# Kernel optimization log

Hardware: AMD Instinct MI355X
Metric: run time of the kernel (lower is better)

The kernel has to match this reference:

```python
import jax, jax.numpy as jnp
import numpy as np

HEADS = 8
DIM_HEAD = 64
WINDOW = 8  # local_window_size


def _sn_weight(W, u, sigma):
    """SNLinear reparameterized weight: one power-iteration step (detached)
    then sigma_W = v^T W u (grad flows through W only), weight = W/sigma_W * sigma."""
    v = W @ u
    v = v / jnp.linalg.norm(v)
    u2 = W.T @ v
    u2 = u2 / jnp.linalg.norm(u2)
    v = jax.lax.stop_gradient(v)
    u2 = jax.lax.stop_gradient(u2)
    sigma_w = jnp.einsum('c,cd,d->', v, W, u2)
    return W / sigma_w * sigma


def setup_inputs() -> dict:
    key = jax.random.key(0)
    ks = jax.random.split(key, 6)
    B, S, D = 2, 2048, 512
    inner = HEADS * DIM_HEAD  # 512
    x = jax.random.normal(ks[0], (B, S, D), dtype=jnp.float32)
    W_qkv = 0.02 * jax.random.normal(ks[1], (3 * inner, D), dtype=jnp.float32)
    u_qkv = jax.random.normal(ks[2], (D,), dtype=jnp.float32)
    u_qkv = u_qkv / jnp.linalg.norm(u_qkv)
    W_out = 0.02 * jax.random.normal(ks[3], (D, inner), dtype=jnp.float32)
    b_out = jnp.zeros((D,), dtype=jnp.float32)
    u_out = jax.random.normal(ks[4], (inner,), dtype=jnp.float32)
    u_out = u_out / jnp.linalg.norm(u_out)
    sigma_qkv = jnp.ones((1,), dtype=jnp.float32)
    sigma_out = jnp.ones((1,), dtype=jnp.float32)
    temperature = jnp.asarray(np.log(DIM_HEAD ** -0.5), dtype=jnp.float32)
    return {
        'x': x, 'W_qkv': W_qkv, 'u_qkv': u_qkv, 'sigma_qkv': sigma_qkv,
        'W_out': W_out, 'b_out': b_out, 'u_out': u_out, 'sigma_out': sigma_out,
        'temperature': temperature,
    }


def reference(x, W_qkv, u_qkv, sigma_qkv, W_out, b_out, u_out, sigma_out, temperature):
    B, S, D = x.shape
    # qkv projection (spectral-normed, no bias)
    Wq = _sn_weight(W_qkv, u_qkv, sigma_qkv[0])
    qkv = x @ Wq.T                                   # [B,S,3*inner]
    q, k, v = jnp.split(qkv, 3, axis=-1)
    to_heads = lambda t: t.reshape(B, S, HEADS, DIM_HEAD).transpose(0, 2, 1, 3)
    q, k, v = to_heads(q), to_heads(k), to_heads(v)   # [B,H,S,Dh]
    dots = jnp.einsum('bhid,bhjd->bhij', q, k) * jnp.exp(temperature)
    # local causal band mask (True inside band); original masked_fill fills True
    i = jnp.arange(S)
    band = (i[:, None] >= i[None, :]) & ((i[:, None] - i[None, :]) <= (WINDOW - 1))
    neg = -jnp.finfo(dots.dtype).max
    dots = jnp.where(band[None, None, :, :], neg, dots)
    attn = jax.nn.softmax(dots, axis=-1)
    out = jnp.einsum('bhij,bhjd->bhid', attn, v)      # [B,H,S,Dh]
    out = out.transpose(0, 2, 1, 3).reshape(B, S, HEADS * DIM_HEAD)
    Wo = _sn_weight(W_out, u_out, sigma_out[0])
    return out @ Wo.T + b_out
```

## Files before the change

kernel.cpp:

```cpp
#include <hip/hip_runtime.h>
#include <hip/hip_bf16.h>
#include <math.h>

#define HEADS 8
#define DH 64
#define SEQ 2048
#define BATCH 2
#define DMODEL 512
#define INNER 512
#define WIN 8

typedef unsigned short ushort_t;
typedef __attribute__((ext_vector_type(8))) __bf16 bf16x8;
typedef __attribute__((ext_vector_type(8))) unsigned short u16x8;
typedef __attribute__((ext_vector_type(4))) float f32x4;

__device__ inline float bf2f(ushort_t u) {
    unsigned v = ((unsigned)u) << 16; float f; __builtin_memcpy(&f, &v, 4); return f;
}
__device__ inline ushort_t f2bf(float f) {
    __hip_bfloat16 h = __float2bfloat16(f); ushort_t u; __builtin_memcpy(&u, &h, 2); return u;
}
__device__ inline int swz_idx(int row, int col) { return ((row << 6) | col) ^ ((row & 7) << 3); }

__device__ inline bf16x8 ld_frag(const ushort_t* lds, int row, int col) {
    u16x8 v = *(const u16x8*)&lds[swz_idx(row, col)];
    return __builtin_bit_cast(bf16x8, v);
}
__device__ inline f32x4 mfma16(bf16x8 a, bf16x8 b, f32x4 c) {
    return __builtin_amdgcn_mfma_f32_16x16x32_bf16(a, b, c, 0, 0, 0);
}
__device__ inline void gload16(const void* g, void* l) {
    __builtin_amdgcn_global_load_lds(
        (const __attribute__((address_space(1))) unsigned int*)g,
        (__attribute__((address_space(3))) unsigned int*)l, 16, 0, 0);
}

__global__ __launch_bounds__(256) void cast_zero_kernel(const float* __restrict__ x,
                                                        const float* __restrict__ Wq,
                                                        const float* __restrict__ Wo,
                                                        ushort_t* __restrict__ xb,
                                                        ushort_t* __restrict__ wqb,
                                                        ushort_t* __restrict__ wob,
                                                        float* __restrict__ zbuf) {
    const int gid = blockIdx.x * 256 + threadIdx.x;
    const float* src; ushort_t* dst; int g;
    if (gid < 262144)      { src = x;  dst = xb;  g = gid; }
    else if (gid < 360448) { src = Wq; dst = wqb; g = gid - 262144; }
    else                   { src = Wo; dst = wob; g = gid - 360448; }
    float4 a = *(const float4*)&src[(size_t)g * 8];
    float4 b = *(const float4*)&src[(size_t)g * 8 + 4];
    u16x8 o;
    o[0] = f2bf(a.x); o[1] = f2bf(a.y); o[2] = f2bf(a.z); o[3] = f2bf(a.w);
    o[4] = f2bf(b.x); o[5] = f2bf(b.y); o[6] = f2bf(b.z); o[7] = f2bf(b.w);
    *(u16x8*)&dst[(size_t)g * 8] = o;
    if (gid < 1024) zbuf[gid] = 0.f;
}

__global__ __launch_bounds__(256) void sn1_kernel(const float* __restrict__ Wq,
                                                  const float* __restrict__ uq,
                                                  const float* __restrict__ Wo,
                                                  const float* __restrict__ uo,
                                                  float* __restrict__ v1,
                                                  float* __restrict__ v2) {
    const int lane = threadIdx.x & 63, w = threadIdx.x >> 6;
    const int r = blockIdx.x * 4 + w;
    const float* W; const float* u; float* vout; int rr;
    if (r < 1536) { W = Wq; u = uq; vout = v1; rr = r; }
    else          { W = Wo; u = uo; vout = v2; rr = r - 1536; }
    float4 w0 = *(const float4*)&W[(size_t)rr * 512 + lane * 8];
    float4 w1 = *(const float4*)&W[(size_t)rr * 512 + lane * 8 + 4];
    float4 u0 = *(const float4*)&u[lane * 8];
    float4 u1 = *(const float4*)&u[lane * 8 + 4];
    float dot = w0.x * u0.x + w0.y * u0.y + w0.z * u0.z + w0.w * u0.w +
                w1.x * u1.x + w1.y * u1.y + w1.z * u1.z + w1.w * u1.w;
#pragma unroll
    for (int off = 1; off < 64; off <<= 1) dot += __shfl_xor(dot, off, 64);
    if (lane == 0) vout[rr] = dot;
}

__global__ __launch_bounds__(256) void sn2_kernel(const float* __restrict__ Wq,
                                                  const float* __restrict__ Wo,
                                                  const float* __restrict__ v1,
                                                  const float* __restrict__ v2,
                                                  float* __restrict__ z1,
                                                  float* __restrict__ z2) {
    const int t = threadIdx.x, b = blockIdx.x;
    const float* W; const float* v; float* z; int r0;
    if (b < 96) { W = Wq; v = v1; z = z1; r0 = b * 16; }
    else        { W = Wo; v = v2; z = z2; r0 = (b - 96) * 16; }
    float a0 = 0.f, a1 = 0.f;
    for (int i = 0; i < 16; ++i) {
        float vv = v[r0 + i];
        a0 += W[(size_t)(r0 + i) * 512 + t] * vv;
        a1 += W[(size_t)(r0 + i) * 512 + 256 + t] * vv;
    }
    atomicAdd(&z[t], a0);
    atomicAdd(&z[t + 256], a1);
}

__global__ __launch_bounds__(256) void sn3_kernel(const float* __restrict__ v1,
                                                  const float* __restrict__ v2,
                                                  const float* __restrict__ z1,
                                                  const float* __restrict__ z2,
                                                  const float* __restrict__ sq,
                                                  const float* __restrict__ so,
                                                  float* __restrict__ scales) {
    __shared__ float red[256];
    const int t = threadIdx.x;
    const float* v; const float* z; const float* sg; int R;
    if (blockIdx.x == 0) { v = v1; z = z1; sg = sq; R = 1536; }
    else                 { v = v2; z = z2; sg = so; R = 512;  }
    float n1 = 0.f;
    for (int i = t; i < R; i += 256) { float x = v[i]; n1 += x * x; }
    red[t] = n1; __syncthreads();
    for (int off = 128; off > 0; off >>= 1) { if (t < off) red[t] += red[t + off]; __syncthreads(); }
    n1 = red[0]; __syncthreads();
    float n2 = 0.f;
    for (int i = t; i < 512; i += 256) { float x = z[i]; n2 += x * x; }
    red[t] = n2; __syncthreads();
    for (int off = 128; off > 0; off >>= 1) { if (t < off) red[t] += red[t + off]; __syncthreads(); }
    if (t == 0) scales[blockIdx.x] = sg[0] * sqrtf(n1 / red[0]);
}

__global__ __launch_bounds__(256) void gemm_bt_qkv(const ushort_t* __restrict__ A,
                                                   const ushort_t* __restrict__ B,
                                                   ushort_t* __restrict__ qkv) {
    constexpr int K = DMODEL;
    __shared__ ushort_t As[8 * 128 * 8];
    __shared__ ushort_t Bs[8 * 128 * 8];
    const int t = threadIdx.x, lane = t & 63, w = t >> 6;
    const int wm = w >> 1, wn = w & 1, lg = lane >> 4, li = lane & 15;
    const int m0 = blockIdx.y * 128, n0 = blockIdx.x * 128;
    f32x4 acc[4][4] = {};
    for (int k0 = 0; k0 < K; k0 += 64) {
        __syncthreads();
#pragma unroll
        for (int i = 0; i < 4; ++i) {
            int j = w * 4 + i;
            int kc = j >> 1, mh = (j & 1) * 64;
            gload16(&A[(size_t)(m0 + mh + lane) * K + k0 + kc * 8], &As[(kc * 128 + mh) * 8]);
            gload16(&B[(size_t)(n0 + mh + lane) * K + k0 + kc * 8], &Bs[(kc * 128 + mh) * 8]);
        }
        __syncthreads();
#pragma unroll
        for (int kw = 0; kw < 2; ++kw) {
            bf16x8 af[4], bf[4];
#pragma unroll
            for (int mi = 0; mi < 4; ++mi)
                af[mi] = *(const bf16x8*)&As[((kw * 4 + lg) * 128 + wm * 64 + mi * 16 + li) * 8];
#pragma unroll
            for (int ni = 0; ni < 4; ++ni)
                bf[ni] = *(const bf16x8*)&Bs[((kw * 4 + lg) * 128 + wn * 64 + ni * 16 + li) * 8];
#pragma unroll
            for (int mi = 0; mi < 4; ++mi)
#pragma unroll
                for (int ni = 0; ni < 4; ++ni)
                    acc[mi][ni] = mfma16(af[mi], bf[ni], acc[mi][ni]);
        }
    }
    ushort_t* vT = qkv + (size_t)2 * BATCH * HEADS * SEQ * DH;
    if (n0 >= 1024) {
#pragma unroll
        for (int mi = 0; mi < 4; ++mi) {
            int base = m0 + wm * 64 + mi * 16 + lg * 4;
            int bb = base >> 11, ss = base & 2047;
#pragma unroll
            for (int ni = 0; ni < 4; ++ni) {
                int n = n0 + wn * 64 + ni * 16 + li;
                int h = (n >> 6) & 7, d0 = n & 63;
                ushort4 o;
                o.x = f2bf(acc[mi][ni][0]); o.y = f2bf(acc[mi][ni][1]);
                o.z = f2bf(acc[mi][ni][2]); o.w = f2bf(acc[mi][ni][3]);
                *(ushort4*)&vT[((size_t)((bb * HEADS + h) * DH) + d0) * SEQ + ss] = o;
            }
        }
    } else {
#pragma unroll
        for (int mi = 0; mi < 4; ++mi)
#pragma unroll
            for (int r = 0; r < 4; ++r) {
                int row = m0 + wm * 64 + mi * 16 + lg * 4 + r;
                int bb = row >> 11, ss = row & 2047;
#pragma unroll
                for (int ni = 0; ni < 4; ++ni) {
                    int n = n0 + wn * 64 + ni * 16 + li;
                    int which = n >> 9, h = (n >> 6) & 7, d0 = n & 63;
                    qkv[(size_t)which * (BATCH * HEADS * SEQ * DH) +
                        ((size_t)((bb * HEADS + h) * SEQ) + ss) * DH + d0] = f2bf(acc[mi][ni][r]);
                }
            }
    }
}

__global__ __launch_bounds__(256) void gemm_bt_out(const ushort_t* __restrict__ A,
                                                   const ushort_t* __restrict__ B,
                                                   const float* __restrict__ scales,
                                                   const float* __restrict__ bias,
                                                   float* __restrict__ C) {
    constexpr int K = INNER;
    __shared__ ushort_t As[8 * 128 * 8];
    __shared__ ushort_t Bs[8 * 128 * 8];
    const int t = threadIdx.x, lane = t & 63, w = t >> 6;
    const int wm = w >> 1, wn = w & 1, lg = lane >> 4, li = lane & 15;
    const int m0 = blockIdx.y * 128, n0 = blockIdx.x * 128;
    f32x4 acc[4][4] = {};
    for (int k0 = 0; k0 < K; k0 += 64) {
        __syncthreads();
#pragma unroll
        for (int i = 0; i < 4; ++i) {
            int j = w * 4 + i;
            int kc = j >> 1, mh = (j & 1) * 64;
            gload16(&A[(size_t)(m0 + mh + lane) * K + k0 + kc * 8], &As[(kc * 128 + mh) * 8]);
            gload16(&B[(size_t)(n0 + mh + lane) * K + k0 + kc * 8], &Bs[(kc * 128 + mh) * 8]);
        }
        __syncthreads();
#pragma unroll
        for (int kw = 0; kw < 2; ++kw) {
            bf16x8 af[4], bf[4];
#pragma unroll
            for (int mi = 0; mi < 4; ++mi)
                af[mi] = *(const bf16x8*)&As[((kw * 4 + lg) * 128 + wm * 64 + mi * 16 + li) * 8];
#pragma unroll
            for (int ni = 0; ni < 4; ++ni)
                bf[ni] = *(const bf16x8*)&Bs[((kw * 4 + lg) * 128 + wn * 64 + ni * 16 + li) * 8];
#pragma unroll
            for (int mi = 0; mi < 4; ++mi)
#pragma unroll
                for (int ni = 0; ni < 4; ++ni)
                    acc[mi][ni] = mfma16(af[mi], bf[ni], acc[mi][ni]);
        }
    }
    const float sc = scales[0] * scales[1];
#pragma unroll
    for (int mi = 0; mi < 4; ++mi)
#pragma unroll
        for (int r = 0; r < 4; ++r) {
            int row = m0 + wm * 64 + mi * 16 + lg * 4 + r;
#pragma unroll
            for (int ni = 0; ni < 4; ++ni) {
                int n = n0 + wn * 64 + ni * 16 + li;
                C[(size_t)row * INNER + n] = acc[mi][ni][r] * sc + bias[n];
            }
        }
}

__global__ __launch_bounds__(512) void attn_mfma_kernel(const ushort_t* __restrict__ qkv,
                                                        const float* __restrict__ temp,
                                                        const float* __restrict__ scales,
                                                        ushort_t* __restrict__ attn_out) {
    __shared__ ushort_t lds[6 * 4096];
    __shared__ float lsr[64];
    const int t    = threadIdx.x;
    const int lane = t & 63, w = t >> 6;
    const int g    = w >> 2, wl = w & 3;
    const int lg   = lane >> 4, li = lane & 15;
    const int bh   = blockIdx.x >> 5;
    const int i0   = (blockIdx.x & 31) * 64;
    const ushort_t* qp  = qkv;
    const ushort_t* kp  = qkv + (size_t)BATCH * HEADS * SEQ * DH;
    const ushort_t* vTp = kp  + (size_t)BATCH * HEADS * SEQ * DH;
    const float s0 = scales[0];
    const float st = expf(temp[0]) * s0 * s0;

    ushort_t* Kb = lds + g * 4096;
    ushort_t* Vb = lds + 8192 + g * 4096;
    ushort_t* Pb = lds + 16384 + g * 4096;

    bf16x8 aQ[2];
#pragma unroll
    for (int c = 0; c < 2; ++c) {
        u16x8 qv = *(const u16x8*)&qp[((size_t)bh * SEQ + i0 + 16 * wl + li) * DH + 32 * c + lg * 8];
        u16x8 r;
#pragma unroll
        for (int j = 0; j < 8; ++j) r[j] = f2bf(bf2f(qv[j]) * st);
        aQ[c] = __builtin_bit_cast(bf16x8, r);
    }

    float lsum[4] = {0.f, 0.f, 0.f, 0.f};
    f32x4 oacc[4] = {};

    for (int jt = 0; jt < SEQ / 128; ++jt) {
        __syncthreads();
        for (int u = t; u < 2048; u += 512) {
            int sel = u >> 9, idx = u & 511;
            int row = idx >> 3, ch = idx & 7;
            int j0s = (2 * jt + (sel & 1)) * 64;
            u16x8 val;
            if (sel < 2) val = *(const u16x8*)&kp[((size_t)bh * SEQ + j0s + row) * DH + ch * 8];
            else         val = *(const u16x8*)&vTp[((size_t)bh * DH + row) * SEQ + j0s + ch * 8];
            ushort_t* dst = lds + ((sel & 2) << 12) + ((sel & 1) << 12);
            *(u16x8*)&dst[swz_idx(row, ch * 8)] = val;
        }
        __syncthreads();

        const int j0 = (2 * jt + g) * 64;
        f32x4 s[4];
#pragma unroll
        for (int kc = 0; kc < 4; ++kc) {
            bf16x8 b0 = ld_frag(Kb, kc * 16 + li, lg * 8);
            bf16x8 b1 = ld_frag(Kb, kc * 16 + li, 32 + lg * 8);
            f32x4 z = {0.f, 0.f, 0.f, 0.f};
            z = mfma16(aQ[0], b0, z);
            z = mfma16(aQ[1], b1, z);
            s[kc] = z;
        }
        const bool need_mask = (j0 == i0) || (j0 == i0 - 64);
        if (need_mask) {
#pragma unroll
            for (int kc = 0; kc < 4; ++kc)
#pragma unroll
                for (int r = 0; r < 4; ++r) {
                    int qi = i0 + 16 * wl + lg * 4 + r;
                    int kj = j0 + kc * 16 + li;
                    float pv = ((unsigned)(qi - kj) < (unsigned)WIN) ? 0.f : __expf(s[kc][r]);
                    lsum[r] += pv;
                    Pb[swz_idx(16 * wl + lg * 4 + r, kc * 16 + li)] = f2bf(pv);
                }
        } else {
#pragma unroll
            for (int kc = 0; kc < 4; ++kc)
#pragma unroll
                for (int r = 0; r < 4; ++r) {
                    float pv = __expf(s[kc][r]);
                    lsum[r] += pv;
                    Pb[swz_idx(16 * wl + lg * 4 + r, kc * 16 + li)] = f2bf(pv);
                }
        }
        bf16x8 aP[2];
#pragma unroll
        for (int c = 0; c < 2; ++c) aP[c] = ld_frag(Pb, 16 * wl + li, c * 32 + lg * 8);
#pragma unroll
        for (int tt = 0; tt < 4; ++tt) {
            bf16x8 b0 = ld_frag(Vb, tt * 16 + li, lg * 8);
            bf16x8 b1 = ld_frag(Vb, tt * 16 + li, 32 + lg * 8);
            oacc[tt] = mfma16(aP[0], b0, oacc[tt]);
            oacc[tt] = mfma16(aP[1], b1, oacc[tt]);
        }
    }
#pragma unroll
    for (int r = 0; r < 4; ++r) {
        float l = lsum[r];
        l += __shfl_xor(l, 1, 16);
        l += __shfl_xor(l, 2, 16);
        l += __shfl_xor(l, 4, 16);
        l += __shfl_xor(l, 8, 16);
        lsum[r] = l;
    }
    float* O_part = (float*)lds;
    __syncthreads();
    if (g == 1) {
#pragma unroll
        for (int r = 0; r < 4; ++r) {
            int row = 16 * wl + lg * 4 + r;
            if (li == 0) lsr[row] = lsum[r];
#pragma unroll
            for (int tt = 0; tt < 4; ++tt)
                O_part[row * 64 + tt * 16 + li] = oacc[tt][r];
        }
    }
    __syncthreads();
    if (g == 0) {
        const int b_ = bh >> 3, h = bh & 7;
#pragma unroll
        for (int r = 0; r < 4; ++r) {
            int row = 16 * wl + lg * 4 + r;
            float inv = 1.0f / (lsum[r] + lsr[row]);
            size_t base = ((size_t)(b_ * SEQ + i0 + row)) * INNER + h * DH;
#pragma unroll
            for (int tt = 0; tt < 4; ++tt)
                attn_out[base + tt * 16 + li] =
                    f2bf((oacc[tt][r] + O_part[row * 64 + tt * 16 + li]) * inv);
        }
    }
}

extern "C" void kernel_launch(void* const* d_in, const int* in_sizes, int n_in,
                              void* d_out, int out_size, void* d_ws, size_t ws_size,
                              hipStream_t stream) {
    const float* x     = (const float*)d_in[0];
    const float* W_qkv = (const float*)d_in[1];
    const float* u_qkv = (const float*)d_in[2];
    const float* s_qkv = (const float*)d_in[3];
    const float* W_out = (const float*)d_in[4];
    const float* b_out = (const float*)d_in[5];
    const float* u_out = (const float*)d_in[6];
    const float* s_out = (const float*)d_in[7];
    const float* temp  = (const float*)d_in[8];
    float* out = (float*)d_out;

    float* scales = (float*)d_ws;
    float* v1 = scales + 64;
    float* v2 = v1 + 1536;
    float* z1 = v2 + 512;
    float* z2 = z1 + 512;
    ushort_t* xb    = (ushort_t*)((char*)d_ws + 16384);
    ushort_t* wqb   = xb + (size_t)2097152;
    ushort_t* wob   = wqb + (size_t)786432;
    ushort_t* qkvb  = wob + (size_t)262144;
    ushort_t* attnb = qkvb + (size_t)6291456;

    cast_zero_kernel<<<dim3(1536), dim3(256), 0, stream>>>(x, W_qkv, W_out, xb, wqb, wob, z1);
    sn1_kernel<<<dim3(512), dim3(256), 0, stream>>>(W_qkv, u_qkv, W_out, u_out, v1, v2);
    sn2_kernel<<<dim3(128), dim3(256), 0, stream>>>(W_qkv, W_out, v1, v2, z1, z2);
    sn3_kernel<<<dim3(2), dim3(256), 0, stream>>>(v1, v2, z1, z2, s_qkv, s_out, scales);
    gemm_bt_qkv<<<dim3(12, 32), dim3(256), 0, stream>>>(xb, wqb, qkvb);
    attn_mfma_kernel<<<dim3(512), dim3(512), 0, stream>>>(qkvb, temp, scales, attnb);
    gemm_bt_out<<<dim3(4, 32), dim3(256), 0, stream>>>(attnb, wob, scales, b_out, out);
}
```

Measured before the change: 173.6 us.

## Fuse spectral-norm prep kernels and double-buffer K/V tiles in attention

```diff
diff --git a/kernel.cpp b/kernel.cpp
--- a/kernel.cpp
+++ b/kernel.cpp
@@ -36,91 +36,97 @@
         (__attribute__((address_space(3))) unsigned int*)l, 16, 0, 0);
 }
 
-__global__ __launch_bounds__(256) void cast_zero_kernel(const float* __restrict__ x,
-                                                        const float* __restrict__ Wq,
-                                                        const float* __restrict__ Wo,
-                                                        ushort_t* __restrict__ xb,
-                                                        ushort_t* __restrict__ wqb,
-                                                        ushort_t* __restrict__ wob,
-                                                        float* __restrict__ zbuf) {
-    const int gid = blockIdx.x * 256 + threadIdx.x;
-    const float* src; ushort_t* dst; int g;
-    if (gid < 262144)      { src = x;  dst = xb;  g = gid; }
-    else if (gid < 360448) { src = Wq; dst = wqb; g = gid - 262144; }
-    else                   { src = Wo; dst = wob; g = gid - 360448; }
-    float4 a = *(const float4*)&src[(size_t)g * 8];
-    float4 b = *(const float4*)&src[(size_t)g * 8 + 4];
-    u16x8 o;
-    o[0] = f2bf(a.x); o[1] = f2bf(a.y); o[2] = f2bf(a.z); o[3] = f2bf(a.w);
-    o[4] = f2bf(b.x); o[5] = f2bf(b.y); o[6] = f2bf(b.z); o[7] = f2bf(b.w);
-    *(u16x8*)&dst[(size_t)g * 8] = o;
-    if (gid < 1024) zbuf[gid] = 0.f;
-}
-
-__global__ __launch_bounds__(256) void sn1_kernel(const float* __restrict__ Wq,
-                                                  const float* __restrict__ uq,
-                                                  const float* __restrict__ Wo,
-                                                  const float* __restrict__ uo,
-                                                  float* __restrict__ v1,
-                                                  float* __restrict__ v2) {
-    const int lane = threadIdx.x & 63, w = threadIdx.x >> 6;
-    const int r = blockIdx.x * 4 + w;
-    const float* W; const float* u; float* vout; int rr;
-    if (r < 1536) { W = Wq; u = uq; vout = v1; rr = r; }
-    else          { W = Wo; u = uo; vout = v2; rr = r - 1536; }
-    float4 w0 = *(const float4*)&W[(size_t)rr * 512 + lane * 8];
-    float4 w1 = *(const float4*)&W[(size_t)rr * 512 + lane * 8 + 4];
-    float4 u0 = *(const float4*)&u[lane * 8];
-    float4 u1 = *(const float4*)&u[lane * 8 + 4];
-    float dot = w0.x * u0.x + w0.y * u0.y + w0.z * u0.z + w0.w * u0.w +
-                w1.x * u1.x + w1.y * u1.y + w1.z * u1.z + w1.w * u1.w;
-#pragma unroll
-    for (int off = 1; off < 64; off <<= 1) dot += __shfl_xor(dot, off, 64);
-    if (lane == 0) vout[rr] = dot;
-}
-
-__global__ __launch_bounds__(256) void sn2_kernel(const float* __restrict__ Wq,
-                                                  const float* __restrict__ Wo,
-                                                  const float* __restrict__ v1,
-                                                  const float* __restrict__ v2,
-                                                  float* __restrict__ z1,
-                                                  float* __restrict__ z2) {
+__global__ __launch_bounds__(256) void fused_cast_sn1(const float* __restrict__ x,
+                                                      const float* __restrict__ Wq,
+                                                      const float* __restrict__ Wo,
+                                                      const float* __restrict__ uq,
+                                                      const float* __restrict__ uo,
+                                                      ushort_t* __restrict__ xb,
+                                                      ushort_t* __restrict__ wqb,
+                                                      ushort_t* __restrict__ wob,
+                                                      float* __restrict__ zbuf,
+                                                      float* __restrict__ v1,
+                                                      float* __restrict__ v2) {
+    const int b = blockIdx.x;
+    if (b < 1536) {
+        const int gid = b * 256 + threadIdx.x;
+        const float* src; ushort_t* dst; int g;
+        if (gid < 262144)      { src = x;  dst = xb;  g = gid; }
+        else if (gid < 360448) { src = Wq; dst = wqb; g = gid - 262144; }
+        else                   { src = Wo; dst = wob; g = gid - 360448; }
+        float4 a = *(const float4*)&src[(size_t)g * 8];
+        float4 c = *(const float4*)&src[(size_t)g * 8 + 4];
+        u16x8 o;
+        o[0] = f2bf(a.x); o[1] = f2bf(a.y); o[2] = f2bf(a.z); o[3] = f2bf(a.w);
+        o[4] = f2bf(c.x); o[5] = f2bf(c.y); o[6] = f2bf(c.z); o[7] = f2bf(c.w);
+        *(u16x8*)&dst[(size_t)g * 8] = o;
+        if (gid < 1032) zbuf[gid] = 0.f;
+    } else {
+        const int lane = threadIdx.x & 63, w = threadIdx.x >> 6;
+        const int r = (b - 1536) * 4 + w;
+        const float* W; const float* u; float* vout; int rr;
+        if (r < 1536) { W = Wq; u = uq; vout = v1; rr = r; }
+        else          { W = Wo; u = uo; vout = v2; rr = r - 1536; }
+        float4 w0 = *(const float4*)&W[(size_t)rr * 512 + lane * 8];
+        float4 w1 = *(const float4*)&W[(size_t)rr * 512 + lane * 8 + 4];
+        float4 u0 = *(const float4*)&u[lane * 8];
+        float4 u1 = *(const float4*)&u[lane * 8 + 4];
+        float dot = w0.x * u0.x + w0.y * u0.y + w0.z * u0.z + w0.w * u0.w +
+                    w1.x * u1.x + w1.y * u1.y + w1.z * u1.z + w1.w * u1.w;
+#pragma unroll
+        for (int off = 1; off < 64; off <<= 1) dot += __shfl_xor(dot, off, 64);
+        if (lane == 0) vout[rr] = dot;
+    }
+}
+
+__global__ __launch_bounds__(256) void fused_sn2_sn3(const float* __restrict__ Wq,
+                                                     const float* __restrict__ Wo,
+                                                     const float* __restrict__ v1,
+                                                     const float* __restrict__ v2,
+                                                     float* __restrict__ z1,
+                                                     float* __restrict__ z2,
+                                                     float* __restrict__ counter,
+                                                     const float* __restrict__ sq,
+                                                     const float* __restrict__ so,
+                                                     float* __restrict__ scales) {
+    __shared__ float red[256];
+    __shared__ int is_last;
     const int t = threadIdx.x, b = blockIdx.x;
-    const float* W; const float* v; float* z; int r0;
-    if (b < 96) { W = Wq; v = v1; z = z1; r0 = b * 16; }
-    else        { W = Wo; v = v2; z = z2; r0 = (b - 96) * 16; }
-    float a0 = 0.f, a1 = 0.f;
-    for (int i = 0; i < 16; ++i) {
-        float vv = v[r0 + i];
-        a0 += W[(size_t)(r0 + i) * 512 + t] * vv;
-        a1 += W[(size_t)(r0 + i) * 512 + 256 + t] * vv;
-    }
-    atomicAdd(&z[t], a0);
-    atomicAdd(&z[t + 256], a1);
-}
-
-__global__ __launch_bounds__(256) void sn3_kernel(const float* __restrict__ v1,
-                                                  const float* __restrict__ v2,
-                                                  const float* __restrict__ z1,
-                                                  const float* __restrict__ z2,
-                                                  const float* __restrict__ sq,
-                                                  const float* __restrict__ so,
-                                                  float* __restrict__ scales) {
-    __shared__ float red[256];
-    const int t = threadIdx.x;
-    const float* v; const float* z; const float* sg; int R;
-    if (blockIdx.x == 0) { v = v1; z = z1; sg = sq; R = 1536; }
-    else                 { v = v2; z = z2; sg = so; R = 512;  }
-    float n1 = 0.f;
-    for (int i = t; i < R; i += 256) { float x = v[i]; n1 += x * x; }
-    red[t] = n1; __syncthreads();
-    for (int off = 128; off > 0; off >>= 1) { if (t < off) red[t] += red[t + off]; __syncthreads(); }
-    n1 = red[0]; __syncthreads();
-    float n2 = 0.f;
-    for (int i = t; i < 512; i += 256) { float x = z[i]; n2 += x * x; }
-    red[t] = n2; __syncthreads();
-    for (int off = 128; off > 0; off >>= 1) { if (t < off) red[t] += red[t + off]; __syncthreads(); }
-    if (t == 0) scales[blockIdx.x] = sg[0] * sqrtf(n1 / red[0]);
+    {
+        const float* W; const float* v; float* z; int r0;
+        if (b < 96) { W = Wq; v = v1; z = z1; r0 = b * 16; }
+        else        { W = Wo; v = v2; z = z2; r0 = (b - 96) * 16; }
+        float a0 = 0.f, a1 = 0.f;
+        for (int i = 0; i < 16; ++i) {
+            float vv = v[r0 + i];
+            a0 += W[(size_t)(r0 + i) * 512 + t] * vv;
+            a1 += W[(size_t)(r0 + i) * 512 + 256 + t] * vv;
+        }
+        atomicAdd(&z[t], a0);
+        atomicAdd(&z[t + 256], a1);
+    }
+    __threadfence();
+    __syncthreads();
+    if (t == 0) is_last = (atomicAdd(counter, 1.0f) == 127.0f);
+    __syncthreads();
+    if (!is_last) return;
+    __threadfence();
+    for (int which = 0; which < 2; ++which) {
+        const float* v = which ? v2 : v1;
+        const float* z = which ? z2 : z1;
+        const int R = which ? 512 : 1536;
+        float n1 = 0.f;
+        for (int i = t; i < R; i += 256) { float q = v[i]; n1 += q * q; }
+        red[t] = n1; __syncthreads();
+        for (int off = 128; off > 0; off >>= 1) { if (t < off) red[t] += red[t + off]; __syncthreads(); }
+        n1 = red[0]; __syncthreads();
+        float n2 = 0.f;
+        for (int i = t; i < 512; i += 256) { float q = z[i]; n2 += q * q; }
+        red[t] = n2; __syncthreads();
+        for (int off = 128; off > 0; off >>= 1) { if (t < off) red[t] += red[t + off]; __syncthreads(); }
+        if (t == 0) scales[which] = (which ? so[0] : sq[0]) * sqrtf(n1 / red[0]);
+        __syncthreads();
+    }
 }
 
 __global__ __launch_bounds__(256) void gemm_bt_qkv(const ushort_t* __restrict__ A,
@@ -249,8 +255,8 @@
                                                         const float* __restrict__ temp,
                                                         const float* __restrict__ scales,
                                                         ushort_t* __restrict__ attn_out) {
-    __shared__ ushort_t lds[6 * 4096];
-    __shared__ float lsr[64];
+    __shared__ ushort_t kvbuf[2 * 4 * 4096];
+    __shared__ ushort_t Pl[2 * 4096];
     const int t    = threadIdx.x;
     const int lane = t & 63, w = t >> 6;
     const int g    = w >> 2, wl = w & 3;
@@ -263,9 +269,11 @@
     const float s0 = scales[0];
     const float st = expf(temp[0]) * s0 * s0;
 
-    ushort_t* Kb = lds + g * 4096;
-    ushort_t* Vb = lds + 8192 + g * 4096;
-    ushort_t* Pb = lds + 16384 + g * 4096;
+    const int srow = t >> 3, sch = (t & 7) * 8;
+    const ushort_t* kbase = kp  + (size_t)bh * SEQ * DH + (size_t)srow * DH + sch;
+    const ushort_t* vbase = vTp + (size_t)bh * DH * SEQ + (size_t)srow * SEQ + sch;
+    const int sdst = swz_idx(srow, sch);
+    ushort_t* Pb = Pl + g * 4096;
 
     bf16x8 aQ[2];
 #pragma unroll
@@ -279,22 +287,35 @@
 
     float lsum[4] = {0.f, 0.f, 0.f, 0.f};
     f32x4 oacc[4] = {};
-
+    u16x8 pre0, pre1, pre2, pre3;
+
+    pre0 = *(const u16x8*)(kbase);
+    pre1 = *(const u16x8*)(kbase + (size_t)64 * DH);
+    pre2 = *(const u16x8*)(vbase);
+    pre3 = *(const u16x8*)(vbase + 64);
+    {
+        ushort_t* bfr = kvbuf;
+        *(u16x8*)&bfr[sdst]         = pre0;
+        *(u16x8*)&bfr[4096 + sdst]  = pre1;
+        *(u16x8*)&bfr[8192 + sdst]  = pre2;
+        *(u16x8*)&bfr[12288 + sdst] = pre3;
+    }
+    __syncthreads();
+
+    int cur = 0;
     for (int jt = 0; jt < SEQ / 128; ++jt) {
-        __syncthreads();
-        for (int u = t; u < 2048; u += 512) {
-            int sel = u >> 9, idx = u & 511;
-            int row = idx >> 3, ch = idx & 7;
-            int j0s = (2 * jt + (sel & 1)) * 64;
-            u16x8 val;
-            if (sel < 2) val = *(const u16x8*)&kp[((size_t)bh * SEQ + j0s + row) * DH + ch * 8];
-            else         val = *(const u16x8*)&vTp[((size_t)bh * DH + row) * SEQ + j0s + ch * 8];
-            ushort_t* dst = lds + ((sel & 2) << 12) + ((sel & 1) << 12);
-            *(u16x8*)&dst[swz_idx(row, ch * 8)] = val;
-        }
-        __syncthreads();
-
-        const int j0 = (2 * jt + g) * 64;
+        if (jt < SEQ / 128 - 1) {
+            const size_t ko = (size_t)(jt + 1) * 128 * DH;
+            const size_t vo = (size_t)(jt + 1) * 128;
+            pre0 = *(const u16x8*)(kbase + ko);
+            pre1 = *(const u16x8*)(kbase + ko + (size_t)64 * DH);
+            pre2 = *(const u16x8*)(vbase + vo);
+            pre3 = *(const u16x8*)(vbase + vo + 64);
+        }
+        const ushort_t* Kb = kvbuf + cur * 16384 + g * 4096;
+        const ushort_t* Vb = kvbuf + cur * 16384 + 8192 + g * 4096;
+        const int j0 = jt * 128 + g * 64;
+
         f32x4 s[4];
 #pragma unroll
         for (int kc = 0; kc < 4; ++kc) {
@@ -337,7 +358,17 @@
             oacc[tt] = mfma16(aP[0], b0, oacc[tt]);
             oacc[tt] = mfma16(aP[1], b1, oacc[tt]);
         }
-    }
+        if (jt < SEQ / 128 - 1) {
+            ushort_t* bfr = kvbuf + (cur ^ 1) * 16384;
+            *(u16x8*)&bfr[sdst]         = pre0;
+            *(u16x8*)&bfr[4096 + sdst]  = pre1;
+            *(u16x8*)&bfr[8192 + sdst]  = pre2;
+            *(u16x8*)&bfr[12288 + sdst] = pre3;
+        }
+        __syncthreads();
+        cur ^= 1;
+    }
+
 #pragma unroll
     for (int r = 0; r < 4; ++r) {
         float l = lsum[r];
@@ -347,8 +378,8 @@
         l += __shfl_xor(l, 8, 16);
         lsum[r] = l;
     }
-    float* O_part = (float*)lds;
-    __syncthreads();
+    float* O_part = (float*)kvbuf;
+    float* lsr    = (float*)Pl;
     if (g == 1) {
 #pragma unroll
         for (int r = 0; r < 4; ++r) {
@@ -356,7 +387,7 @@
             if (li == 0) lsr[row] = lsum[r];
 #pragma unroll
             for (int tt = 0; tt < 4; ++tt)
-                O_part[row * 64 + tt * 16 + li] = oacc[tt][r];
+                O_part[row * 68 + tt * 16 + li] = oacc[tt][r];
         }
     }
     __syncthreads();
@@ -370,7 +401,7 @@
 #pragma unroll
             for (int tt = 0; tt < 4; ++tt)
                 attn_out[base + tt * 16 + li] =
-                    f2bf((oacc[tt][r] + O_part[row * 64 + tt * 16 + li]) * inv);
+                    f2bf((oacc[tt][r] + O_part[row * 68 + tt * 16 + li]) * inv);
         }
     }
 }
@@ -389,21 +420,22 @@
     const float* temp  = (const float*)d_in[8];
     float* out = (float*)d_out;
 
-    float* scales = (float*)d_ws;
-    float* v1 = scales + 64;
-    float* v2 = v1 + 1536;
-    float* z1 = v2 + 512;
-    float* z2 = z1 + 512;
+    float* scales  = (float*)d_ws;
+    float* v1      = scales + 64;
+    float* v2      = v1 + 1536;
+    float* z1      = v2 + 512;
+    float* z2      = z1 + 512;
+    float* counter = z1 + 1024;
     ushort_t* xb    = (ushort_t*)((char*)d_ws + 16384);
     ushort_t* wqb   = xb + (size_t)2097152;
     ushort_t* wob   = wqb + (size_t)786432;
     ushort_t* qkvb  = wob + (size_t)262144;
     ushort_t* attnb = qkvb + (size_t)6291456;
 
-    cast_zero_kernel<<<dim3(1536), dim3(256), 0, stream>>>(x, W_qkv, W_out, xb, wqb, wob, z1);
-    sn1_kernel<<<dim3(512), dim3(256), 0, stream>>>(W_qkv, u_qkv, W_out, u_out, v1, v2);
-    sn2_kernel<<<dim3(128), dim3(256), 0, stream>>>(W_qkv, W_out, v1, v2, z1, z2);
-    sn3_kernel<<<dim3(2), dim3(256), 0, stream>>>(v1, v2, z1, z2, s_qkv, s_out, scales);
+    fused_cast_sn1<<<dim3(2048), dim3(256), 0, stream>>>(x, W_qkv, W_out, u_qkv, u_out,
+                                                         xb, wqb, wob, z1, v1, v2);
+    fused_sn2_sn3<<<dim3(128), dim3(256), 0, stream>>>(W_qkv, W_out, v1, v2, z1, z2,
+                                                       counter, s_qkv, s_out, scales);
     gemm_bt_qkv<<<dim3(12, 32), dim3(256), 0, stream>>>(xb, wqb, qkvb);
     attn_mfma_kernel<<<dim3(512), dim3(512), 0, stream>>>(qkvb, temp, scales, attnb);
     gemm_bt_out<<<dim3(4, 32), dim3(256), 0, stream>>>(attnb, wob, scales, b_out, out);
```

Result: faster. 166.2 us (-4.3%).
